# Kernel optimization log

Measured on AMD Instinct MI355X. Metric: run time of the kernel, lower is better.

The kernel has to match this reference:

```python
import jax, jax.numpy as jnp
import numpy as np

DIM = 256
HEADS = 4
HEAD_DIM = DIM // HEADS
SCALE = HEAD_DIM ** -0.5


def setup_inputs() -> dict:
    key = jax.random.key(0)
    k_x, k_wqkv, k_bqkv, k_wp, k_bp = jax.random.split(key, 5)
    B, N = 8, 2048
    x = jax.random.normal(k_x, (B, N, DIM), dtype=jnp.float32)
    # torch nn.Linear weights: [out_features, in_features]
    W_qkv = jax.random.normal(k_wqkv, (3 * DIM, DIM), dtype=jnp.float32) * (DIM ** -0.5)
    b_qkv = jax.random.normal(k_bqkv, (3 * DIM,), dtype=jnp.float32) * 0.02
    W_proj = jax.random.normal(k_wp, (DIM, DIM), dtype=jnp.float32) * (DIM ** -0.5)
    b_proj = jax.random.normal(k_bp, (DIM,), dtype=jnp.float32) * 0.02
    return {"x": x, "W_qkv": W_qkv, "b_qkv": b_qkv, "W_proj": W_proj, "b_proj": b_proj}


def reference(x, W_qkv, b_qkv, W_proj, b_proj):
    B, N, C = x.shape
    h, d = HEADS, HEAD_DIM
    # fused QKV projection: [B,N,3C] -> [3,B,h,N,d]
    qkv = (jnp.einsum('bnc,oc->bno', x, W_qkv) + b_qkv)
    qkv = qkv.reshape(B, N, 3, h, d).transpose(2, 0, 3, 1, 4)
    q, k, v = qkv[0], qkv[1], qkv[2]
    # full N x N score matrix, as in the original module
    attn = jnp.einsum('bhnd,bhmd->bhnm', q, k) * SCALE
    attn = jax.nn.softmax(attn, axis=-1)
    out = jnp.einsum('bhnm,bhmd->bhnd', attn, v)  # [B,h,N,d]
    out = out.transpose(0, 2, 1, 3).reshape(B, N, C)
    return jnp.einsum('bnc,oc->bno', out, W_proj) + b_proj
```

## Files before the change

kernel.cpp:

```cpp
#include <hip/hip_runtime.h>
#include <hip/hip_bf16.h>


typedef __bf16 bf16x8 __attribute__((ext_vector_type(8)));
typedef float f32x4 __attribute__((ext_vector_type(4)));
typedef float f32x16 __attribute__((ext_vector_type(16)));
typedef unsigned u32x2 __attribute__((ext_vector_type(2)));

#define MFMA16(a, b, c) __builtin_amdgcn_mfma_f32_16x16x32_bf16((a), (b), (c), 0, 0, 0)
#define MFMA32(a, b, c) __builtin_amdgcn_mfma_f32_32x32x16_bf16((a), (b), (c), 0, 0, 0)

#define C2 0.18033688011112042f

__device__ __forceinline__ bf16x8 ldg8(const __bf16* p) {
    return *reinterpret_cast<const bf16x8*>(p);
}

__device__ __forceinline__ bf16x8 cvt8(const float* p) {
    const f32x4 a = *reinterpret_cast<const f32x4*>(p);
    const f32x4 b = *reinterpret_cast<const f32x4*>(p + 4);
    bf16x8 r;
    r[0] = (__bf16)a[0]; r[1] = (__bf16)a[1]; r[2] = (__bf16)a[2]; r[3] = (__bf16)a[3];
    r[4] = (__bf16)b[0]; r[5] = (__bf16)b[1]; r[6] = (__bf16)b[2]; r[7] = (__bf16)b[3];
    return r;
}

__device__ __forceinline__ unsigned pk2(float a, float b) {
    __bf16 x = (__bf16)a, y = (__bf16)b;
    unsigned short ux = __builtin_bit_cast(unsigned short, x);
    unsigned short uy = __builtin_bit_cast(unsigned short, y);
    return (unsigned)ux | ((unsigned)uy << 16);
}

__global__ __launch_bounds__(256) void cvt_all(
    const float* __restrict__ X, const float* __restrict__ Wq,
    const float* __restrict__ Wp, __bf16* __restrict__ Xb,
    __bf16* __restrict__ Wqb, __bf16* __restrict__ Wpb)
{
    const int g = blockIdx.x * 256 + threadIdx.x;
    const float* src;
    __bf16* dst;
    int off;
    if (g < 524288)      { src = X;  dst = Xb;  off = g; }
    else if (g < 548864) { src = Wq; dst = Wqb; off = g - 524288; }
    else                 { src = Wp; dst = Wpb; off = g - 548864; }
    *reinterpret_cast<bf16x8*>(dst + (size_t)off * 8) = cvt8(src + (size_t)off * 8);
}

__global__ __launch_bounds__(256) void qkv_gemm(
    const __bf16* __restrict__ X, const __bf16* __restrict__ Wq,
    const float* __restrict__ bq, __bf16* __restrict__ Qw,
    __bf16* __restrict__ Kw, __bf16* __restrict__ Vt)
{
    const int tid = threadIdx.x;
    const int w = tid >> 6, lane = tid & 63;
    const int lo = lane & 15, hi = lane >> 4;
    const int n0 = blockIdx.x * 128;
    const int m0 = blockIdx.y * 128 + w * 32;

    f32x4 acc[2][8] = {};
    const __bf16* xp = X + (m0 + lo) * 256 + hi * 8;
    const __bf16* wp = Wq + (n0 + lo) * 256 + hi * 8;
    #pragma unroll
    for (int k = 0; k < 256; k += 32) {
        bf16x8 a0 = ldg8(xp + k);
        bf16x8 a1 = ldg8(xp + 16 * 256 + k);
        #pragma unroll
        for (int f = 0; f < 8; ++f) {
            bf16x8 bf = ldg8(wp + f * 16 * 256 + k);
            acc[0][f] = MFMA16(a0, bf, acc[0][f]);
            acc[1][f] = MFMA16(a1, bf, acc[1][f]);
        }
    }

    #pragma unroll
    for (int ni = 0; ni < 8; ++ni) {
        const int col = n0 + ni * 16 + lo;
        const float bias = bq[col];
        const float scale = (col < 256) ? C2 : 1.0f;
        #pragma unroll
        for (int mi = 0; mi < 2; ++mi) {
            #pragma unroll
            for (int r = 0; r < 4; ++r) {
                const int row = m0 + mi * 16 + hi * 4 + r;
                const __bf16 hv = (__bf16)((acc[mi][ni][r] + bias) * scale);
                const int bb = row >> 11, n = row & 2047;
                const int d = col & 63;
                if (col < 256) {
                    const int h = col >> 6;
                    Qw[((bb * 4 + h) * 2048 + n) * 64 + d] = hv;
                } else if (col < 512) {
                    const int h = (col - 256) >> 6;
                    Kw[((bb * 4 + h) * 2048 + n) * 64 + d] = hv;
                } else {
                    const int h = (col - 512) >> 6;
                    Vt[((bb * 4 + h) * 64 + d) * 2048 + n] = hv;
                }
            }
        }
    }
}

__global__ __launch_bounds__(1024, 2) void attn_kernel(
    const __bf16* __restrict__ Qw, const __bf16* __restrict__ Kw,
    const __bf16* __restrict__ Vt, __bf16* __restrict__ Ow)
{
    __shared__ __align__(16) char lds[65536];

    const int tid = threadIdx.x;
    const int w = tid >> 6, lane = tid & 63;
    const int l31 = lane & 31, hi5 = lane >> 5;
    const int sw = w & 3;
    const int g  = w >> 2;

    const int bid = blockIdx.x;
    const int work = (bid & 7) * 64 + (bid >> 3);
    const int bh = work >> 4;
    const int qx = work & 15;

    const int q = qx * 128 + sw * 32 + l31;
    const int kvbase = g * 512;
    const int gbase = g * 16384;

    const __bf16* Qp = Qw + (bh * 2048 + q) * 64 + hi5 * 8;
    bf16x8 Qf[4];
    #pragma unroll
    for (int db = 0; db < 4; ++db) Qf[db] = ldg8(Qp + db * 16);

    const __bf16* Kbase = Kw + (size_t)bh * 2048 * 64;
    const __bf16* Vbase = Vt + (size_t)bh * 64 * 2048;

    const int idx = tid & 255;
    const int krow = idx >> 3, kcol8 = (idx & 7) * 8;
    const int swz = ((idx >> 3) & 7) << 4;
    const int kb0 = gbase + ((idx * 16) ^ swz);
    const int kb1 = gbase + (((idx + 256) * 16) ^ swz);
    const int vb0 = gbase + 8192 + ((idx * 16) ^ swz);
    const int vb1 = gbase + 8192 + (((idx + 256) * 16) ^ swz);

    bf16x8 R0 = ldg8(Kbase + (kvbase + krow) * 64 + kcol8);
    bf16x8 R1 = ldg8(Kbase + (kvbase + krow + 32) * 64 + kcol8);
    bf16x8 R2 = ldg8(Vbase + krow * 2048 + kvbase + kcol8);
    bf16x8 R3 = ldg8(Vbase + (krow + 32) * 2048 + kvbase + kcol8);

    f32x16 oacc0 = (f32x16)0.0f, oacc1 = (f32x16)0.0f;
    float lr = 0.0f;

    for (int t = 0; t < 8; ++t) {
        *reinterpret_cast<bf16x8*>(lds + kb0) = R0;
        *reinterpret_cast<bf16x8*>(lds + kb1) = R1;
        *reinterpret_cast<bf16x8*>(lds + vb0) = R2;
        *reinterpret_cast<bf16x8*>(lds + vb1) = R3;
        __syncthreads();

        if (t < 7) {
            const int kv0n = kvbase + (t + 1) * 64;
            R0 = ldg8(Kbase + (kv0n + krow) * 64 + kcol8);
            R1 = ldg8(Kbase + (kv0n + krow + 32) * 64 + kcol8);
            R2 = ldg8(Vbase + krow * 2048 + kv0n + kcol8);
            R3 = ldg8(Vbase + (krow + 32) * 2048 + kv0n + kcol8);
        }

        f32x16 s0 = (f32x16)0.0f, s1 = (f32x16)0.0f;
        #pragma unroll
        for (int db = 0; db < 4; ++db) {
            const int colb = hi5 * 16 + db * 32;
            bf16x8 k0 = *reinterpret_cast<const bf16x8*>(
                lds + gbase + ((l31 * 128 + colb) ^ ((l31 & 7) << 4)));
            bf16x8 k1 = *reinterpret_cast<const bf16x8*>(
                lds + gbase + (((l31 + 32) * 128 + colb) ^ ((l31 & 7) << 4)));
            s0 = MFMA32(k0, Qf[db], s0);
            s1 = MFMA32(k1, Qf[db], s1);
        }

        float p0[16], p1[16];
        #pragma unroll
        for (int i = 0; i < 16; ++i) p0[i] = exp2f(s0[i]);
        #pragma unroll
        for (int i = 0; i < 16; ++i) p1[i] = exp2f(s1[i]);

        float r0 = 0.f, r1 = 0.f, r2 = 0.f, r3 = 0.f;
        #pragma unroll
        for (int i = 0; i < 4; ++i) {
            r0 += p0[i]; r1 += p0[4 + i]; r2 += p0[8 + i]; r3 += p0[12 + i];
            r0 += p1[i]; r1 += p1[4 + i]; r2 += p1[8 + i]; r3 += p1[12 + i];
        }
        lr += (r0 + r1) + (r2 + r3);

#define PVSTEP(PARR, KH)                                                      \
        {                                                                     \
            _Pragma("unroll")                                                 \
            for (int bb2 = 0; bb2 < 2; ++bb2) {                               \
                const int vcolb = KH * 64 + bb2 * 32 + hi5 * 16;              \
                bf16x8 v0 = *reinterpret_cast<const bf16x8*>(                 \
                    lds + gbase + 8192 + ((l31 * 128 + vcolb) ^ ((l31 & 7) << 4))); \
                bf16x8 v1 = *reinterpret_cast<const bf16x8*>(                 \
                    lds + gbase + 8192 + (((l31 + 32) * 128 + vcolb) ^ ((l31 & 7) << 4))); \
                unsigned w0 = pk2(PARR[8 * bb2 + 0], PARR[8 * bb2 + 1]);      \
                unsigned w1 = pk2(PARR[8 * bb2 + 2], PARR[8 * bb2 + 3]);      \
                unsigned w2 = pk2(PARR[8 * bb2 + 4], PARR[8 * bb2 + 5]);      \
                unsigned w3 = pk2(PARR[8 * bb2 + 6], PARR[8 * bb2 + 7]);      \
                asm volatile("v_permlane32_swap_b32 %0, %1" : "+v"(w0), "+v"(w2)); \
                asm volatile("v_permlane32_swap_b32 %0, %1" : "+v"(w1), "+v"(w3)); \
                union { unsigned u[4]; bf16x8 v; } pb;                        \
                pb.u[0] = w0; pb.u[1] = w1; pb.u[2] = w2; pb.u[3] = w3;       \
                oacc0 = MFMA32(v0, pb.v, oacc0);                              \
                oacc1 = MFMA32(v1, pb.v, oacc1);                              \
            }                                                                 \
        }
        PVSTEP(p0, 0)
        PVSTEP(p1, 1)
#undef PVSTEP
        __syncthreads();
    }

    lr += __shfl_xor(lr, 32);

    __bf16* mb = reinterpret_cast<__bf16*>(lds);
    float*  lb = reinterpret_cast<float*>(lds + 32768);
    const int half = g >> 1;
    const int abase = half * 8192;

#define MWRITE(BASE, LIDX)                                                    \
    {                                                                         \
        _Pragma("unroll")                                                     \
        for (int i = 0; i < 16; ++i) {                                        \
            const int r = (i & 3) + 8 * (i >> 2) + 4 * hi5;                   \
            mb[(BASE) + (sw * 64 + r) * 32 + l31] = (__bf16)oacc0[i];         \
            mb[(BASE) + (sw * 64 + 32 + r) * 32 + l31] = (__bf16)oacc1[i];    \
        }                                                                     \
        if (hi5 == 0) lb[(LIDX) * 128 + sw * 32 + l31] = lr;                  \
    }
#define MACC(BASE, LIDX)                                                      \
    {                                                                         \
        _Pragma("unroll")                                                     \
        for (int i = 0; i < 16; ++i) {                                        \
            const int r = (i & 3) + 8 * (i >> 2) + 4 * hi5;                   \
            oacc0[i] += (float)mb[(BASE) + (sw * 64 + r) * 32 + l31];         \
            oacc1[i] += (float)mb[(BASE) + (sw * 64 + 32 + r) * 32 + l31];    \
        }                                                                     \
        lr += lb[(LIDX) * 128 + sw * 32 + l31];                               \
    }

    if (g & 1) MWRITE(abase, half);
    __syncthreads();
    if (!(g & 1)) MACC(abase, half);
    __syncthreads();
    if (g == 2) MWRITE(0, 0);
    __syncthreads();
    if (g == 0) {
        MACC(0, 0);
        const float invl = 1.0f / lr;
        const int bb = bh >> 2, h = bh & 3;
        __bf16* Op = Ow + ((size_t)(bb * 2048 + q)) * 256 + h * 64 + hi5 * 4;
#define EPI(OACC, DBLK)                                                       \
        {                                                                     \
            _Pragma("unroll")                                                 \
            for (int rq = 0; rq < 4; ++rq) {                                  \
                u32x2 st;                                                     \
                st.x = pk2(OACC[rq * 4 + 0] * invl, OACC[rq * 4 + 1] * invl); \
                st.y = pk2(OACC[rq * 4 + 2] * invl, OACC[rq * 4 + 3] * invl); \
                *reinterpret_cast<u32x2*>(Op + DBLK * 32 + rq * 8) = st;      \
            }                                                                 \
        }
        EPI(oacc0, 0)
        EPI(oacc1, 1)
#undef EPI
    }
#undef MWRITE
#undef MACC
}

__global__ __launch_bounds__(256) void proj_gemm(
    const __bf16* __restrict__ A, const __bf16* __restrict__ Wp,
    const float* __restrict__ bp, float* __restrict__ out)
{
    const int tid = threadIdx.x;
    const int w = tid >> 6, lane = tid & 63;
    const int lo = lane & 15, hi = lane >> 4;
    const int n0 = blockIdx.x * 128;
    const int m0 = blockIdx.y * 128 + w * 32;

    f32x4 acc[2][8] = {};
    const __bf16* ap = A + (m0 + lo) * 256 + hi * 8;
    const __bf16* wp = Wp + (n0 + lo) * 256 + hi * 8;
    #pragma unroll
    for (int k = 0; k < 256; k += 32) {
        bf16x8 a0 = ldg8(ap + k);
        bf16x8 a1 = ldg8(ap + 16 * 256 + k);
        #pragma unroll
        for (int f = 0; f < 8; ++f) {
            bf16x8 bf = ldg8(wp + f * 16 * 256 + k);
            acc[0][f] = MFMA16(a0, bf, acc[0][f]);
            acc[1][f] = MFMA16(a1, bf, acc[1][f]);
        }
    }
    #pragma unroll
    for (int ni = 0; ni < 8; ++ni) {
        const int col = n0 + ni * 16 + lo;
        const float bias = bp[col];
        #pragma unroll
        for (int mi = 0; mi < 2; ++mi) {
            #pragma unroll
            for (int r = 0; r < 4; ++r) {
                const int row = m0 + mi * 16 + hi * 4 + r;
                out[row * 256 + col] = acc[mi][ni][r] + bias;
            }
        }
    }
}

extern "C" void kernel_launch(void* const* d_in, const int* in_sizes, int n_in,
                              void* d_out, int out_size, void* d_ws, size_t ws_size,
                              hipStream_t stream)
{
    const float* x  = (const float*)d_in[0];
    const float* Wq = (const float*)d_in[1];
    const float* bq = (const float*)d_in[2];
    const float* Wp = (const float*)d_in[3];
    const float* bp = (const float*)d_in[4];

    __bf16* ws = (__bf16*)d_ws;
    const size_t SZ = (size_t)32 * 2048 * 64;
    __bf16* Xb  = ws;
    __bf16* Wqb = Xb + SZ;
    __bf16* Wpb = Wqb + 196608;
    __bf16* Qw  = Wpb + 65536;
    __bf16* Kw  = Qw + SZ;
    __bf16* Vt  = Kw + SZ;
    __bf16* Ow  = Xb;

    cvt_all<<<2176, 256, 0, stream>>>(x, Wq, Wp, Xb, Wqb, Wpb);
    qkv_gemm<<<dim3(6, 128), 256, 0, stream>>>(Xb, Wqb, bq, Qw, Kw, Vt);
    attn_kernel<<<512, 1024, 0, stream>>>(Qw, Kw, Vt, Ow);
    proj_gemm<<<dim3(2, 128), 256, 0, stream>>>(Ow, Wpb, bp, (float*)d_out);
}
```

Measured before the change: 142.9 us.

## Stage V transpose through LDS, remap GEMM blocks per XCD, use native exp2

In the QKV GEMM, the V output tiles are now transposed through a swizzled shared-memory buffer, so they can be written to the transposed V layout with 16-byte coalesced stores instead of scattered 2-byte stores. Both GEMMs switch to a 1D grid whose block index is remapped so that consecutive row tiles share an XCD, aiming for better L2 reuse of the X/A rows. The attention softmax replaces exp2f with the hardware v_exp_f32 builtin to avoid the library range-handling code. The costs are 32KB of LDS and a barrier in the V blocks, plus slightly reduced exp2 accuracy for extreme inputs.

```diff
diff --git a/kernel.cpp b/kernel.cpp
--- a/kernel.cpp
+++ b/kernel.cpp
@@ -11,6 +11,16 @@
 #define MFMA32(a, b, c) __builtin_amdgcn_mfma_f32_32x32x16_bf16((a), (b), (c), 0, 0, 0)
 
 #define C2 0.18033688011112042f
+
+#if __has_builtin(__builtin_amdgcn_exp2f)
+__device__ __forceinline__ float fexp2(float x) { return __builtin_amdgcn_exp2f(x); }
+#else
+__device__ __forceinline__ float fexp2(float x) {
+    float r;
+    asm("v_exp_f32 %0, %1" : "=v"(r) : "v"(x));
+    return r;
+}
+#endif
 
 __device__ __forceinline__ bf16x8 ldg8(const __bf16* p) {
     return *reinterpret_cast<const bf16x8*>(p);
@@ -52,11 +62,18 @@
     const float* __restrict__ bq, __bf16* __restrict__ Qw,
     __bf16* __restrict__ Kw, __bf16* __restrict__ Vt)
 {
+    __shared__ __align__(16) char lds[32768];
+
     const int tid = threadIdx.x;
     const int w = tid >> 6, lane = tid & 63;
     const int lo = lane & 15, hi = lane >> 4;
-    const int n0 = blockIdx.x * 128;
-    const int m0 = blockIdx.y * 128 + w * 32;
+
+    const int bid = blockIdx.x;
+    const int xcd = bid & 7, wl = bid >> 3;
+    const int by = xcd * 16 + wl / 6;
+    const int bx = wl % 6;
+    const int n0 = bx * 128;
+    const int m0 = by * 128 + w * 32;
 
     f32x4 acc[2][8] = {};
     const __bf16* xp = X + (m0 + lo) * 256 + hi * 8;
@@ -73,30 +90,56 @@
         }
     }
 
-    #pragma unroll
-    for (int ni = 0; ni < 8; ++ni) {
-        const int col = n0 + ni * 16 + lo;
-        const float bias = bq[col];
-        const float scale = (col < 256) ? C2 : 1.0f;
-        #pragma unroll
-        for (int mi = 0; mi < 2; ++mi) {
+    if (n0 < 512) {
+        #pragma unroll
+        for (int ni = 0; ni < 8; ++ni) {
+            const int col = n0 + ni * 16 + lo;
+            const float bias = bq[col];
+            const float scale = (col < 256) ? C2 : 1.0f;
             #pragma unroll
-            for (int r = 0; r < 4; ++r) {
-                const int row = m0 + mi * 16 + hi * 4 + r;
-                const __bf16 hv = (__bf16)((acc[mi][ni][r] + bias) * scale);
-                const int bb = row >> 11, n = row & 2047;
-                const int d = col & 63;
-                if (col < 256) {
-                    const int h = col >> 6;
-                    Qw[((bb * 4 + h) * 2048 + n) * 64 + d] = hv;
-                } else if (col < 512) {
-                    const int h = (col - 256) >> 6;
-                    Kw[((bb * 4 + h) * 2048 + n) * 64 + d] = hv;
-                } else {
-                    const int h = (col - 512) >> 6;
-                    Vt[((bb * 4 + h) * 64 + d) * 2048 + n] = hv;
+            for (int mi = 0; mi < 2; ++mi) {
+                #pragma unroll
+                for (int r = 0; r < 4; ++r) {
+                    const int row = m0 + mi * 16 + hi * 4 + r;
+                    const __bf16 hv = (__bf16)((acc[mi][ni][r] + bias) * scale);
+                    const int bb = row >> 11, n = row & 2047;
+                    const int d = col & 63;
+                    if (col < 256) {
+                        const int h = col >> 6;
+                        Qw[((bb * 4 + h) * 2048 + n) * 64 + d] = hv;
+                    } else {
+                        const int h = (col - 256) >> 6;
+                        Kw[((bb * 4 + h) * 2048 + n) * 64 + d] = hv;
+                    }
                 }
             }
+        }
+    } else {
+        #pragma unroll
+        for (int ni = 0; ni < 8; ++ni) {
+            const int cl = ni * 16 + lo;
+            const float bias = bq[n0 + cl];
+            #pragma unroll
+            for (int mi = 0; mi < 2; ++mi) {
+                const int nl2 = (w * 32 + mi * 16 + hi * 4) * 2;
+                u32x2 st;
+                st.x = pk2(acc[mi][ni][0] + bias, acc[mi][ni][1] + bias);
+                st.y = pk2(acc[mi][ni][2] + bias, acc[mi][ni][3] + bias);
+                *reinterpret_cast<u32x2*>(lds + cl * 256 + (nl2 ^ ((cl & 7) << 4))) = st;
+            }
+        }
+        __syncthreads();
+        const int cl = tid >> 1, half = tid & 1;
+        const int vcol = (n0 - 512) + cl;
+        const int h = vcol >> 6, d = vcol & 63;
+        const int bb = by >> 4;
+        const int nbase = (by & 15) * 128 + half * 64;
+        __bf16* dst = Vt + ((size_t)((bb * 4 + h) * 64 + d)) * 2048 + nbase;
+        #pragma unroll
+        for (int c = 0; c < 8; ++c) {
+            const int byte = cl * 256 + ((half * 128 + c * 16) ^ ((cl & 7) << 4));
+            *reinterpret_cast<bf16x8*>(dst + c * 8) =
+                *reinterpret_cast<const bf16x8*>(lds + byte);
         }
     }
 }
@@ -175,9 +218,9 @@
 
         float p0[16], p1[16];
         #pragma unroll
-        for (int i = 0; i < 16; ++i) p0[i] = exp2f(s0[i]);
-        #pragma unroll
-        for (int i = 0; i < 16; ++i) p1[i] = exp2f(s1[i]);
+        for (int i = 0; i < 16; ++i) p0[i] = fexp2(s0[i]);
+        #pragma unroll
+        for (int i = 0; i < 16; ++i) p1[i] = fexp2(s1[i]);
 
         float r0 = 0.f, r1 = 0.f, r2 = 0.f, r3 = 0.f;
         #pragma unroll
@@ -278,8 +321,13 @@
     const int tid = threadIdx.x;
     const int w = tid >> 6, lane = tid & 63;
     const int lo = lane & 15, hi = lane >> 4;
-    const int n0 = blockIdx.x * 128;
-    const int m0 = blockIdx.y * 128 + w * 32;
+
+    const int bid = blockIdx.x;
+    const int xcd = bid & 7, wl = bid >> 3;
+    const int by = xcd * 16 + (wl >> 1);
+    const int bx = wl & 1;
+    const int n0 = bx * 128;
+    const int m0 = by * 128 + w * 32;
 
     f32x4 acc[2][8] = {};
     const __bf16* ap = A + (m0 + lo) * 256 + hi * 8;
@@ -331,7 +379,7 @@
     __bf16* Ow  = Xb;
 
     cvt_all<<<2176, 256, 0, stream>>>(x, Wq, Wp, Xb, Wqb, Wpb);
-    qkv_gemm<<<dim3(6, 128), 256, 0, stream>>>(Xb, Wqb, bq, Qw, Kw, Vt);
+    qkv_gemm<<<768, 256, 0, stream>>>(Xb, Wqb, bq, Qw, Kw, Vt);
     attn_kernel<<<512, 1024, 0, stream>>>(Qw, Kw, Vt, Ow);
-    proj_gemm<<<dim3(2, 128), 256, 0, stream>>>(Ow, Wpb, bp, (float*)d_out);
-}
+    proj_gemm<<<256, 256, 0, stream>>>(Ow, Wpb, bp, (float*)d_out);
+}
```

New measurement: 148.0 us. 3.6% more time.
